# Kernel optimization log

Measured on AMD Instinct MI355X. Metric: run time of the kernel, lower is better.

## Reference

```python
import jax, jax.numpy as jnp
import numpy as np

D_MODEL = 1024
D_HEAD = 64


def setup_inputs() -> dict:
    key = jax.random.key(0)
    k_x, k_q, k_k, k_v, k_o = jax.random.split(key, 5)
    scale = 1.0 / np.sqrt(D_MODEL)
    residual_stream = jax.random.normal(k_x, (4, 2048, D_MODEL), dtype=jnp.float32)
    Q = scale * jax.random.normal(k_q, (D_MODEL, D_HEAD), dtype=jnp.float32)
    K = scale * jax.random.normal(k_k, (D_MODEL, D_HEAD), dtype=jnp.float32)
    V = scale * jax.random.normal(k_v, (D_MODEL, D_HEAD), dtype=jnp.float32)
    O = scale * jax.random.normal(k_o, (D_MODEL, D_HEAD), dtype=jnp.float32)
    return {"residual_stream": residual_stream, "Q": Q, "K": K, "V": V, "O": O}


def reference(residual_stream, Q, K, V, O) -> jnp.ndarray:
    # queries/keys: [B, S, d_head]
    queries = jnp.einsum('bsd,dh->bsh', residual_stream, Q)
    keys = jnp.einsum('bsd,dh->bsh', residual_stream, K)
    # NOTE: original module applies NO 1/sqrt(d_head) scaling.
    pre_attention = jnp.einsum('bqh,bkh->bqk', queries, keys)  # [B, S, S]
    S = pre_attention.shape[-1]
    causal = jnp.tril(jnp.ones((S, S), dtype=bool))
    pre_attention = jnp.where(causal[None], pre_attention, -jnp.inf)
    attention = jax.nn.softmax(pre_attention, axis=-1)
    # x = residual @ V @ O^T : [B, S, d_model]
    x = jnp.einsum('bsd,dh,eh->bse', residual_stream, V, O)
    return jnp.einsum('bqk,bke->bqe', attention, x)
```

## Files before the change

### kernel.cpp

```cpp
#include <hip/hip_runtime.h>
#include <hip/hip_bf16.h>
#include <math.h>

#define BATCH 4
#define SEQ   2048
#define DM    1024
#define DH    64
#define NROWS (BATCH*SEQ)

typedef __hip_bfloat16 bf16;
typedef __attribute__((ext_vector_type(8))) short short8;
typedef __attribute__((ext_vector_type(8))) unsigned short ushortx8;
typedef __attribute__((ext_vector_type(4))) float floatx4;

__device__ __forceinline__ ushort f2bf(float f) {
    union { bf16 h; ushort u; } cv;
    cv.h = __float2bfloat16(f);
    return cv.u;
}
__device__ __forceinline__ float bf2f(ushort u) {
    union { unsigned int i; float f; } v; v.i = ((unsigned int)u) << 16; return v.f;
}

__device__ __forceinline__ void load_lds16(const ushort* g, ushort* l) {
    __builtin_amdgcn_global_load_lds(
        (const __attribute__((address_space(1))) unsigned int*)g,
        (__attribute__((address_space(3))) unsigned int*)l, 16, 0, 0);
}

__global__ __launch_bounds__(256) void wprep_kernel(
    const float* __restrict__ Q, const float* __restrict__ K,
    const float* __restrict__ V, const float* __restrict__ O,
    ushort* __restrict__ WhT, ushort* __restrict__ WlT,
    ushort* __restrict__ Oh, ushort* __restrict__ Ol)
{
    int n = blockIdx.x;
    if (n < 192) {
        const float* W = (n < 64) ? Q : (n < 128) ? K : V;
        int c = n & 63;
        for (int k = threadIdx.x; k < DM; k += 256) {
            float w = W[k * DH + c];
            ushort hi = f2bf(w);
            WhT[n * DM + k] = hi;
            WlT[n * DM + k] = f2bf(w - bf2f(hi));
        }
    } else {
        int e0 = (n - 192) << 4;
        for (int idx = threadIdx.x; idx < 16 * DH; idx += 256) {
            int off = (e0 << 6) + idx;
            float w = O[off];
            ushort hi = f2bf(w);
            Oh[off] = hi;
            Ol[off] = f2bf(w - bf2f(hi));
        }
    }
}

__global__ __launch_bounds__(256) void qkv_part_kernel(
    const float* __restrict__ x, const ushort* __restrict__ WhT,
    const ushort* __restrict__ WlT, float* __restrict__ Cpart)
{
    __shared__ __align__(16) ushort Xs[2][32][34];
    __shared__ __align__(16) ushort Ws[2][192][34];
    int s0 = blockIdx.x * 32;
    int kb = blockIdx.y * 256;
    int t = threadIdx.x;
    int wave = t >> 6, lane = t & 63, m_ = lane & 15, qd = lane >> 4;
    const floatx4 z4 = {0.f, 0.f, 0.f, 0.f};
    floatx4 accq[2] = {z4, z4}, acck[2] = {z4, z4}, accv[2] = {z4, z4};
    int xr = t >> 3, xc = (t & 7) * 4;
    for (int k0 = 0; k0 < 256; k0 += 32) {
        float4 v = *(const float4*)&x[(size_t)(s0 + xr) * DM + kb + k0 + xc];
        ushort h0 = f2bf(v.x), h1 = f2bf(v.y), h2 = f2bf(v.z), h3 = f2bf(v.w);
        *(ushort4*)&Xs[0][xr][xc] = make_ushort4(h0, h1, h2, h3);
        *(ushort4*)&Xs[1][xr][xc] = make_ushort4(
            f2bf(v.x - bf2f(h0)), f2bf(v.y - bf2f(h1)),
            f2bf(v.z - bf2f(h2)), f2bf(v.w - bf2f(h3)));
        #pragma unroll
        for (int j = 0; j < 3; ++j) {
            int idx = t + j * 256, n = idx >> 2, kc = (idx & 3) * 8;
            *(uint4*)&Ws[0][n][kc] = *(const uint4*)&WhT[n * DM + kb + k0 + kc];
            *(uint4*)&Ws[1][n][kc] = *(const uint4*)&WlT[n * DM + kb + k0 + kc];
        }
        __syncthreads();
        short8 ah[2], al[2];
        #pragma unroll
        for (int mi = 0; mi < 2; ++mi) {
            ah[mi] = *(const short8*)&Xs[0][mi * 16 + m_][qd * 8];
            al[mi] = *(const short8*)&Xs[1][mi * 16 + m_][qd * 8];
        }
        int nq = wave * 16 + m_, nk = 64 + wave * 16 + m_, nv = 128 + wave * 16 + m_;
        short8 bqh = *(const short8*)&Ws[0][nq][qd * 8];
        short8 bql = *(const short8*)&Ws[1][nq][qd * 8];
        short8 bkh = *(const short8*)&Ws[0][nk][qd * 8];
        short8 bkl = *(const short8*)&Ws[1][nk][qd * 8];
        short8 bvh = *(const short8*)&Ws[0][nv][qd * 8];
        #pragma unroll
        for (int mi = 0; mi < 2; ++mi) {
            accq[mi] = __builtin_amdgcn_mfma_f32_16x16x32_bf16(ah[mi], bqh, accq[mi], 0, 0, 0);
            accq[mi] = __builtin_amdgcn_mfma_f32_16x16x32_bf16(al[mi], bqh, accq[mi], 0, 0, 0);
            accq[mi] = __builtin_amdgcn_mfma_f32_16x16x32_bf16(ah[mi], bql, accq[mi], 0, 0, 0);
            acck[mi] = __builtin_amdgcn_mfma_f32_16x16x32_bf16(ah[mi], bkh, acck[mi], 0, 0, 0);
            acck[mi] = __builtin_amdgcn_mfma_f32_16x16x32_bf16(al[mi], bkh, acck[mi], 0, 0, 0);
            acck[mi] = __builtin_amdgcn_mfma_f32_16x16x32_bf16(ah[mi], bkl, acck[mi], 0, 0, 0);
            accv[mi] = __builtin_amdgcn_mfma_f32_16x16x32_bf16(ah[mi], bvh, accv[mi], 0, 0, 0);
        }
        __syncthreads();
    }
    float* Cp = Cpart + (size_t)blockIdx.y * (NROWS * 192);
    #pragma unroll
    for (int mi = 0; mi < 2; ++mi) {
        #pragma unroll
        for (int r = 0; r < 4; ++r) {
            int row = s0 + mi * 16 + qd * 4 + r;
            float* base = Cp + (size_t)row * 192;
            base[wave * 16 + m_]       = accq[mi][r];
            base[64 + wave * 16 + m_]  = acck[mi][r];
            base[128 + wave * 16 + m_] = accv[mi][r];
        }
    }
}

__global__ __launch_bounds__(256) void qkv_reduce_kernel(
    const float* __restrict__ Cpart,
    ushort* __restrict__ qh, ushort* __restrict__ ql,
    ushort* __restrict__ kh, ushort* __restrict__ kl, ushort* __restrict__ xvP)
{
    __shared__ ushort xvs[32][72];
    const size_t SL = (size_t)NROWS * 192;
    int row0 = blockIdx.x * 32;
    int t = threadIdx.x;
    #pragma unroll
    for (int i = 0; i < 24; ++i) {
        int e = i * 256 + t;
        int r = e / 192, c = e - r * 192;
        size_t row = row0 + r;
        size_t off = row * 192 + c;
        float s = Cpart[off] + Cpart[SL + off] + Cpart[2 * SL + off] + Cpart[3 * SL + off];
        ushort hi = f2bf(s);
        if (c < 64) {
            qh[row * 64 + c] = hi; ql[row * 64 + c] = f2bf(s - bf2f(hi));
        } else if (c < 128) {
            kh[row * 64 + c - 64] = hi; kl[row * 64 + c - 64] = f2bf(s - bf2f(hi));
        } else {
            xvs[r][c - 128] = hi;
        }
    }
    __syncthreads();
    int h = t & 63, qd = t >> 6;
    ushortx8 v;
    #pragma unroll
    for (int j = 0; j < 8; ++j)
        v[j] = xvs[4 * qd + (j & 3) + ((j >> 2) << 4)][h];
    int b = row0 >> 11, c32 = (row0 & 2047) >> 5;
    *(ushortx8*)&xvP[((((size_t)b << 6) + c32) * 4 + qd) * 512 + h * 8] = v;
}

__global__ __launch_bounds__(512) void attn_kernel(
    const ushort* __restrict__ qh, const ushort* __restrict__ ql,
    const ushort* __restrict__ kh, const ushort* __restrict__ kl,
    const ushort* __restrict__ xvP,
    const ushort* __restrict__ Oh, const ushort* __restrict__ Ol,
    float* __restrict__ out)
{
    __shared__ __align__(16) ushort Kbuf[2][8192];
    __shared__ __align__(16) ushort xvbuf[2][4096];
    __shared__ float LO[2][16][68];
    __shared__ float lred[2][2][16];
    __shared__ float lsc[2][16];
    int pp = blockIdx.x & 63, b = blockIdx.x >> 6;
    int srowA = pp << 4, srowB = (127 - pp) << 4;
    int t = threadIdx.x, wave = t >> 6, lane = t & 63, m_ = lane & 15, qd = lane >> 4;
    int nA = (pp >> 2) + 1, nB = ((127 - pp) >> 2) + 1;
    int tile = wave >> 2, h2 = (wave >> 1) & 1, nh = wave & 1;
    int srow = tile ? srowB : srowA;
    int nT = tile ? nB : nA;
    const ushort* khb = kh + (((size_t)b << 11)) * 64;
    const ushort* klb = kl + (((size_t)b << 11)) * 64;
    const ushort* xvPb = xvP + ((size_t)b << 17);
    short8 bq[2][2];
    {
        size_t qr = (size_t)((b << 11) + srow + m_) * 64 + qd * 8;
        bq[0][0] = *(const short8*)&qh[qr];
        bq[0][1] = *(const short8*)&qh[qr + 32];
        bq[1][0] = *(const short8*)&ql[qr];
        bq[1][1] = *(const short8*)&ql[qr + 32];
    }
    int drow = lane >> 3;
    int dlc = ((lane & 7) ^ drow) * 8;
    #define AT_STAGE(cc, buf)                                                   \
        { int k0r_ = (cc) << 6;                                                 \
          _Pragma("unroll")                                                     \
          for (int i_ = 0; i_ < 3; ++i_) {                                      \
              int c_ = wave * 3 + i_;                                           \
              if (c_ < 8)                                                       \
                  load_lds16(khb + (size_t)(k0r_ + c_ * 8 + drow) * 64 + dlc,   \
                             &Kbuf[buf][c_ * 512]);                             \
              else if (c_ < 16)                                                 \
                  load_lds16(klb + (size_t)(k0r_ + (c_ - 8) * 8 + drow) * 64 + dlc, \
                             &Kbuf[buf][4096 + (c_ - 8) * 512]);                \
              else                                                              \
                  load_lds16(xvPb + (size_t)(cc) * 4096 + (c_ - 16) * 512 + lane * 8, \
                             &xvbuf[buf][(c_ - 16) * 512]);                     \
          } }
    const floatx4 z4 = {0.f, 0.f, 0.f, 0.f};
    floatx4 accO[2] = {z4, z4};
    float ll = 0.f;
    int qrow = srow + m_;
    AT_STAGE(0, 0)
    for (int c = 0; c < nB; ++c) {
        __syncthreads();
        if (c + 1 < nB) AT_STAGE(c + 1, (c + 1) & 1)
        if (c < nT) {
            int bufi = c & 1;
            floatx4 accS[2] = {z4, z4};
            #pragma unroll
            for (int kk = 0; kk < 2; ++kk) {
                #pragma unroll
                for (int tt = 0; tt < 2; ++tt) {
                    int row = (2 * h2 + tt) * 16 + m_;
                    int chunk = ((kk << 2) + qd) ^ (m_ & 7);
                    const ushort* ph = &Kbuf[bufi][row * 64 + chunk * 8];
                    short8 akh = *(const short8*)ph;
                    short8 akl = *(const short8*)(ph + 4096);
                    accS[tt] = __builtin_amdgcn_mfma_f32_16x16x32_bf16(akh, bq[0][kk], accS[tt], 0, 0, 0);
                    accS[tt] = __builtin_amdgcn_mfma_f32_16x16x32_bf16(akl, bq[0][kk], accS[tt], 0, 0, 0);
                    accS[tt] = __builtin_amdgcn_mfma_f32_16x16x32_bf16(akh, bq[1][kk], accS[tt], 0, 0, 0);
                }
            }
            float lsum = 0.f;
            short8 pa;
            #pragma unroll
            for (int tt = 0; tt < 2; ++tt) {
                #pragma unroll
                for (int r = 0; r < 4; ++r) {
                    int kc = c * 64 + (2 * h2 + tt) * 16 + qd * 4 + r;
                    float p = (kc <= qrow) ? __expf(accS[tt][r]) : 0.f;
                    lsum += p;
                    pa[tt * 4 + r] = (short)f2bf(p);
                }
            }
            if (nh == 0) ll += lsum;
            const ushort* Xb = &xvbuf[bufi][(h2 * 4 + qd) * 512];
            #pragma unroll
            for (int i = 0; i < 2; ++i) {
                int h = (nh * 2 + i) * 16 + m_;
                short8 xv = *(const short8*)&Xb[h * 8];
                accO[i] = __builtin_amdgcn_mfma_f32_16x16x32_bf16(pa, xv, accO[i], 0, 0, 0);
            }
        }
    }
    ll += __shfl_xor(ll, 16); ll += __shfl_xor(ll, 32);
    if (qd == 0 && nh == 0) lred[tile][h2][m_] = ll;
    #pragma unroll
    for (int h2r = 0; h2r < 2; ++h2r) {
        if (h2 == h2r) {
            #pragma unroll
            for (int i = 0; i < 2; ++i)
                #pragma unroll
                for (int r = 0; r < 4; ++r) {
                    int q = qd * 4 + r, h = (nh * 2 + i) * 16 + m_;
                    if (h2r == 0) LO[tile][q][h] = accO[i][r];
                    else          LO[tile][q][h] += accO[i][r];
                }
        }
        __syncthreads();
    }
    if (t < 32) {
        int tl = t >> 4, q = t & 15;
        lsc[tl][q] = 1.f / (lred[tl][0][q] + lred[tl][1][q]);
    }
    __syncthreads();
    int e0w = wave << 7;
    short8 Ah[2][2], Al[2][2];
    #pragma unroll
    for (int tl = 0; tl < 2; ++tl) {
        float sc = lsc[tl][m_];
        #pragma unroll
        for (int kk = 0; kk < 2; ++kk) {
            #pragma unroll
            for (int j = 0; j < 8; ++j) {
                int h = kk * 32 + qd * 8 + j;
                float v = LO[tl][m_][h] * sc;
                ushort hv = f2bf(v);
                Ah[tl][kk][j] = (short)hv;
                Al[tl][kk][j] = (short)f2bf(v - bf2f(hv));
            }
        }
    }
    floatx4 accE[2][8];
    #pragma unroll
    for (int tl = 0; tl < 2; ++tl)
        #pragma unroll
        for (int ni = 0; ni < 8; ++ni) accE[tl][ni] = z4;
    #pragma unroll
    for (int ni = 0; ni < 8; ++ni) {
        #pragma unroll
        for (int kk = 0; kk < 2; ++kk) {
            size_t boff = (size_t)(e0w + ni * 16 + m_) * 64 + kk * 32 + qd * 8;
            short8 bh = *(const short8*)&Oh[boff];
            short8 bl = *(const short8*)&Ol[boff];
            #pragma unroll
            for (int tl = 0; tl < 2; ++tl) {
                accE[tl][ni] = __builtin_amdgcn_mfma_f32_16x16x32_bf16(Ah[tl][kk], bh, accE[tl][ni], 0, 0, 0);
                accE[tl][ni] = __builtin_amdgcn_mfma_f32_16x16x32_bf16(Al[tl][kk], bh, accE[tl][ni], 0, 0, 0);
                accE[tl][ni] = __builtin_amdgcn_mfma_f32_16x16x32_bf16(Ah[tl][kk], bl, accE[tl][ni], 0, 0, 0);
            }
        }
    }
    float* ob = out + ((size_t)b * SEQ) * DM;
    #pragma unroll
    for (int tl = 0; tl < 2; ++tl) {
        int srw = tl ? srowB : srowA;
        #pragma unroll
        for (int r = 0; r < 4; ++r) {
            float* orow = ob + (size_t)(srw + qd * 4 + r) * DM + e0w;
            #pragma unroll
            for (int ni = 0; ni < 8; ++ni)
                orow[ni * 16 + m_] = accE[tl][ni][r];
        }
    }
    #undef AT_STAGE
}

extern "C" void kernel_launch(void* const* d_in, const int* in_sizes, int n_in,
                              void* d_out, int out_size, void* d_ws, size_t ws_size,
                              hipStream_t stream) {
    const float* x = (const float*)d_in[0];
    const float* Q = (const float*)d_in[1];
    const float* K = (const float*)d_in[2];
    const float* V = (const float*)d_in[3];
    const float* O = (const float*)d_in[4];
    float* out = (float*)d_out;

    char* ws = (char*)d_ws;
    ushort* qh   = (ushort*)(ws);
    ushort* ql   = (ushort*)(ws + (1ull  << 20));
    ushort* kh   = (ushort*)(ws + (2ull  << 20));
    ushort* kl   = (ushort*)(ws + (3ull  << 20));
    ushort* xvP  = (ushort*)(ws + (4ull  << 20));
    ushort* WhT  = (ushort*)(ws + (5ull  << 20));
    ushort* WlT  = (ushort*)(ws + (5ull  << 20) + (512ull << 10));
    ushort* Oh   = (ushort*)(ws + (6ull  << 20));
    ushort* Ol   = (ushort*)(ws + (6ull  << 20) + (128ull << 10));
    float*  Cpart = (float*)(ws + (23ull << 20));

    wprep_kernel<<<256, 256, 0, stream>>>(Q, K, V, O, WhT, WlT, Oh, Ol);
    qkv_part_kernel<<<dim3(NROWS / 32, 4), 256, 0, stream>>>(x, WhT, WlT, Cpart);
    qkv_reduce_kernel<<<NROWS / 32, 256, 0, stream>>>(Cpart, qh, ql, kh, kl, xvP);
    attn_kernel<<<64 * BATCH, 512, 0, stream>>>(qh, ql, kh, kl, xvP, Oh, Ol, out);
}
```

Before: 164.6 us.

## Split attention over key chunks and move output projection to separate kernels

The attention kernel now interleaves its key/value chunks across four split blocks per query-tile pair, so the grid grows from 256 to 1024 blocks. Each block writes unnormalized partial outputs and row sums to workspace. A new reduce kernel sums the eight partials, normalizes, and splits the result into bf16 hi/lo parts. A separate tiled MFMA kernel then applies the O projection. This targets the long serial per-block loop and low occupancy, at the cost of extra workspace traffic (about 16 MB of fp32 partials) and two more launches.

```diff
diff --git a/kernel.cpp b/kernel.cpp
--- a/kernel.cpp
+++ b/kernel.cpp
@@ -7,6 +7,7 @@
 #define DM    1024
 #define DH    64
 #define NROWS (BATCH*SEQ)
+#define PVSPLIT 8
 
 typedef __hip_bfloat16 bf16;
 typedef __attribute__((ext_vector_type(8))) short short8;
@@ -156,25 +157,24 @@
     *(ushortx8*)&xvP[((((size_t)b << 6) + c32) * 4 + qd) * 512 + h * 8] = v;
 }
 
-__global__ __launch_bounds__(512) void attn_kernel(
+__global__ __launch_bounds__(512) void attn_part_kernel(
     const ushort* __restrict__ qh, const ushort* __restrict__ ql,
     const ushort* __restrict__ kh, const ushort* __restrict__ kl,
     const ushort* __restrict__ xvP,
-    const ushort* __restrict__ Oh, const ushort* __restrict__ Ol,
-    float* __restrict__ out)
+    float* __restrict__ Opart, float* __restrict__ lpart)
 {
     __shared__ __align__(16) ushort Kbuf[2][8192];
     __shared__ __align__(16) ushort xvbuf[2][4096];
-    __shared__ float LO[2][16][68];
     __shared__ float lred[2][2][16];
-    __shared__ float lsc[2][16];
-    int pp = blockIdx.x & 63, b = blockIdx.x >> 6;
+    int bid = blockIdx.x;
+    int pp = bid & 63, b = (bid >> 6) & 3, s = bid >> 8;
     int srowA = pp << 4, srowB = (127 - pp) << 4;
     int t = threadIdx.x, wave = t >> 6, lane = t & 63, m_ = lane & 15, qd = lane >> 4;
     int nA = (pp >> 2) + 1, nB = ((127 - pp) >> 2) + 1;
     int tile = wave >> 2, h2 = (wave >> 1) & 1, nh = wave & 1;
     int srow = tile ? srowB : srowA;
     int nT = tile ? nB : nA;
+    int jB = (nB - s + 3) >> 2;
     const ushort* khb = kh + (((size_t)b << 11)) * 64;
     const ushort* klb = kl + (((size_t)b << 11)) * 64;
     const ushort* xvPb = xvP + ((size_t)b << 17);
@@ -207,12 +207,13 @@
     floatx4 accO[2] = {z4, z4};
     float ll = 0.f;
     int qrow = srow + m_;
-    AT_STAGE(0, 0)
-    for (int c = 0; c < nB; ++c) {
+    AT_STAGE(s, 0)
+    for (int j = 0; j < jB; ++j) {
+        int c = s + 4 * j;
         __syncthreads();
-        if (c + 1 < nB) AT_STAGE(c + 1, (c + 1) & 1)
+        if (j + 1 < jB) AT_STAGE(s + 4 * (j + 1), (j + 1) & 1)
         if (c < nT) {
-            int bufi = c & 1;
+            int bufi = j & 1;
             floatx4 accS[2] = {z4, z4};
             #pragma unroll
             for (int kk = 0; kk < 2; ++kk) {
@@ -252,75 +253,103 @@
     }
     ll += __shfl_xor(ll, 16); ll += __shfl_xor(ll, 32);
     if (qd == 0 && nh == 0) lred[tile][h2][m_] = ll;
-    #pragma unroll
-    for (int h2r = 0; h2r < 2; ++h2r) {
-        if (h2 == h2r) {
-            #pragma unroll
-            for (int i = 0; i < 2; ++i)
-                #pragma unroll
-                for (int r = 0; r < 4; ++r) {
-                    int q = qd * 4 + r, h = (nh * 2 + i) * 16 + m_;
-                    if (h2r == 0) LO[tile][q][h] = accO[i][r];
-                    else          LO[tile][q][h] += accO[i][r];
-                }
-        }
-        __syncthreads();
-    }
+    __syncthreads();
     if (t < 32) {
         int tl = t >> 4, q = t & 15;
-        lsc[tl][q] = 1.f / (lred[tl][0][q] + lred[tl][1][q]);
+        int row = (b << 11) + (tl ? srowB : srowA) + q;
+        lpart[(size_t)s * NROWS + row] = lred[tl][0][q] + lred[tl][1][q];
+    }
+    float* OP = Opart + ((size_t)(s * 2 + h2) * NROWS + (b << 11) + srow) * 64;
+    #pragma unroll
+    for (int i = 0; i < 2; ++i)
+        #pragma unroll
+        for (int r = 0; r < 4; ++r)
+            OP[(qd * 4 + r) * 64 + (nh * 2 + i) * 16 + m_] = accO[i][r];
+    #undef AT_STAGE
+}
+
+__global__ __launch_bounds__(256) void axv_reduce_kernel(
+    const float* __restrict__ AxvPart, const float* __restrict__ lpart,
+    ushort* __restrict__ Axvh, ushort* __restrict__ Axvl)
+{
+    const size_t PSL = (size_t)NROWS * DH;
+    int idx = blockIdx.x * 256 + threadIdx.x;
+    size_t e = (size_t)idx * 4;
+    int r = (int)(e >> 6);
+    float4 a = *(const float4*)&AxvPart[e];
+    #pragma unroll
+    for (int sp = 1; sp < PVSPLIT; ++sp) {
+        float4 v = *(const float4*)&AxvPart[sp * PSL + e];
+        a.x += v.x; a.y += v.y; a.z += v.z; a.w += v.w;
+    }
+    float sc = 1.f / (lpart[r] + lpart[NROWS + r]
+                    + lpart[2 * NROWS + r] + lpart[3 * NROWS + r]);
+    a.x *= sc; a.y *= sc; a.z *= sc; a.w *= sc;
+    ushort h0 = f2bf(a.x), h1 = f2bf(a.y), h2 = f2bf(a.z), h3 = f2bf(a.w);
+    *(ushort4*)&Axvh[e] = make_ushort4(h0, h1, h2, h3);
+    *(ushort4*)&Axvl[e] = make_ushort4(
+        f2bf(a.x - bf2f(h0)), f2bf(a.y - bf2f(h1)),
+        f2bf(a.z - bf2f(h2)), f2bf(a.w - bf2f(h3)));
+}
+
+__global__ __launch_bounds__(256) void out_kernel(
+    const ushort* __restrict__ Axvh, const ushort* __restrict__ Axvl,
+    const ushort* __restrict__ Oh, const ushort* __restrict__ Ol,
+    float* __restrict__ out)
+{
+    __shared__ __align__(16) ushort As[2][64][72];
+    __shared__ __align__(16) ushort Bsh[2][128][72];
+    int bid = blockIdx.x;
+    int r0 = (bid >> 3) << 6;
+    int e0 = (bid & 7) << 7;
+    int t = threadIdx.x;
+    {
+        int tr = t >> 2, tc = (t & 3) << 4;
+        const ushort* ah = Axvh + (size_t)(r0 + tr) * DH + tc;
+        const ushort* al = Axvl + (size_t)(r0 + tr) * DH + tc;
+        *(uint4*)&As[0][tr][tc]     = *(const uint4*)ah;
+        *(uint4*)&As[0][tr][tc + 8] = *(const uint4*)(ah + 8);
+        *(uint4*)&As[1][tr][tc]     = *(const uint4*)al;
+        *(uint4*)&As[1][tr][tc + 8] = *(const uint4*)(al + 8);
+    }
+    {
+        int tr = t >> 1, tc = (t & 1) << 5;
+        const ushort* bh = Oh + (size_t)(e0 + tr) * DH + tc;
+        const ushort* bl = Ol + (size_t)(e0 + tr) * DH + tc;
+        *(uint4*)&Bsh[0][tr][tc]      = *(const uint4*)bh;
+        *(uint4*)&Bsh[0][tr][tc + 8]  = *(const uint4*)(bh + 8);
+        *(uint4*)&Bsh[0][tr][tc + 16] = *(const uint4*)(bh + 16);
+        *(uint4*)&Bsh[0][tr][tc + 24] = *(const uint4*)(bh + 24);
+        *(uint4*)&Bsh[1][tr][tc]      = *(const uint4*)bl;
+        *(uint4*)&Bsh[1][tr][tc + 8]  = *(const uint4*)(bl + 8);
+        *(uint4*)&Bsh[1][tr][tc + 16] = *(const uint4*)(bl + 16);
+        *(uint4*)&Bsh[1][tr][tc + 24] = *(const uint4*)(bl + 24);
     }
     __syncthreads();
-    int e0w = wave << 7;
-    short8 Ah[2][2], Al[2][2];
-    #pragma unroll
-    for (int tl = 0; tl < 2; ++tl) {
-        float sc = lsc[tl][m_];
-        #pragma unroll
-        for (int kk = 0; kk < 2; ++kk) {
-            #pragma unroll
-            for (int j = 0; j < 8; ++j) {
-                int h = kk * 32 + qd * 8 + j;
-                float v = LO[tl][m_][h] * sc;
-                ushort hv = f2bf(v);
-                Ah[tl][kk][j] = (short)hv;
-                Al[tl][kk][j] = (short)f2bf(v - bf2f(hv));
-            }
-        }
-    }
-    floatx4 accE[2][8];
-    #pragma unroll
-    for (int tl = 0; tl < 2; ++tl)
-        #pragma unroll
-        for (int ni = 0; ni < 8; ++ni) accE[tl][ni] = z4;
-    #pragma unroll
-    for (int ni = 0; ni < 8; ++ni) {
-        #pragma unroll
-        for (int kk = 0; kk < 2; ++kk) {
-            size_t boff = (size_t)(e0w + ni * 16 + m_) * 64 + kk * 32 + qd * 8;
-            short8 bh = *(const short8*)&Oh[boff];
-            short8 bl = *(const short8*)&Ol[boff];
-            #pragma unroll
-            for (int tl = 0; tl < 2; ++tl) {
-                accE[tl][ni] = __builtin_amdgcn_mfma_f32_16x16x32_bf16(Ah[tl][kk], bh, accE[tl][ni], 0, 0, 0);
-                accE[tl][ni] = __builtin_amdgcn_mfma_f32_16x16x32_bf16(Al[tl][kk], bh, accE[tl][ni], 0, 0, 0);
-                accE[tl][ni] = __builtin_amdgcn_mfma_f32_16x16x32_bf16(Ah[tl][kk], bl, accE[tl][ni], 0, 0, 0);
-            }
-        }
-    }
-    float* ob = out + ((size_t)b * SEQ) * DM;
-    #pragma unroll
-    for (int tl = 0; tl < 2; ++tl) {
-        int srw = tl ? srowB : srowA;
-        #pragma unroll
-        for (int r = 0; r < 4; ++r) {
-            float* orow = ob + (size_t)(srw + qd * 4 + r) * DM + e0w;
-            #pragma unroll
-            for (int ni = 0; ni < 8; ++ni)
-                orow[ni * 16 + m_] = accE[tl][ni][r];
-        }
-    }
-    #undef AT_STAGE
+    int wave = t >> 6, lane = t & 63, m_ = lane & 15, qd = lane >> 4;
+    const floatx4 z4 = {0.f, 0.f, 0.f, 0.f};
+    floatx4 acc[8] = {z4, z4, z4, z4, z4, z4, z4, z4};
+    #pragma unroll
+    for (int kk = 0; kk < 2; ++kk) {
+        short8 ah = *(const short8*)&As[0][wave * 16 + m_][kk * 32 + qd * 8];
+        short8 al = *(const short8*)&As[1][wave * 16 + m_][kk * 32 + qd * 8];
+        #pragma unroll
+        for (int ni = 0; ni < 8; ++ni) {
+            short8 bh = *(const short8*)&Bsh[0][ni * 16 + m_][kk * 32 + qd * 8];
+            short8 bl = *(const short8*)&Bsh[1][ni * 16 + m_][kk * 32 + qd * 8];
+            acc[ni] = __builtin_amdgcn_mfma_f32_16x16x32_bf16(ah, bh, acc[ni], 0, 0, 0);
+            acc[ni] = __builtin_amdgcn_mfma_f32_16x16x32_bf16(al, bh, acc[ni], 0, 0, 0);
+            acc[ni] = __builtin_amdgcn_mfma_f32_16x16x32_bf16(ah, bl, acc[ni], 0, 0, 0);
+        }
+    }
+    #pragma unroll
+    for (int r = 0; r < 4; ++r) {
+        int row = r0 + wave * 16 + qd * 4 + r;
+        float* orow = out + (size_t)row * DM + e0;
+        #pragma unroll
+        for (int ni = 0; ni < 8; ++ni)
+            orow[ni * 16 + m_] = acc[ni][r];
+    }
 }
 
 extern "C" void kernel_launch(void* const* d_in, const int* in_sizes, int n_in,
@@ -341,12 +370,18 @@
     ushort* xvP  = (ushort*)(ws + (4ull  << 20));
     ushort* WhT  = (ushort*)(ws + (5ull  << 20));
     ushort* WlT  = (ushort*)(ws + (5ull  << 20) + (512ull << 10));
-    ushort* Oh   = (ushort*)(ws + (6ull  << 20));
-    ushort* Ol   = (ushort*)(ws + (6ull  << 20) + (128ull << 10));
+    float*  lpart = (float*)(ws + (6ull  << 20));
+    ushort* Oh   = (ushort*)(ws + (6ull  << 20) + (256ull << 10));
+    ushort* Ol   = (ushort*)(ws + (6ull  << 20) + (384ull << 10));
+    float*  Opart = (float*)(ws + (7ull << 20));
     float*  Cpart = (float*)(ws + (23ull << 20));
+    ushort* Axvh = qh;
+    ushort* Axvl = ql;
 
     wprep_kernel<<<256, 256, 0, stream>>>(Q, K, V, O, WhT, WlT, Oh, Ol);
     qkv_part_kernel<<<dim3(NROWS / 32, 4), 256, 0, stream>>>(x, WhT, WlT, Cpart);
     qkv_reduce_kernel<<<NROWS / 32, 256, 0, stream>>>(Cpart, qh, ql, kh, kl, xvP);
-    attn_kernel<<<64 * BATCH, 512, 0, stream>>>(qh, ql, kh, kl, xvP, Oh, Ol, out);
-}
+    attn_part_kernel<<<64 * BATCH * 4, 512, 0, stream>>>(qh, ql, kh, kl, xvP, Opart, lpart);
+    axv_reduce_kernel<<<NROWS * DH / 4 / 256, 256, 0, stream>>>(Opart, lpart, Axvh, Axvl);
+    out_kernel<<<(NROWS / 64) * 8, 256, 0, stream>>>(Axvh, Axvl, Oh, Ol, out);
+}
```

Result: faster. 160.2 us (-2.7%).
